# Optimization experiments

Measured on AMD Instinct MI355X. Metric: run time of the kernel, lower is better.

The kernel has to match this reference:

```python
import jax, jax.numpy as jnp
import numpy as np

B = 8            # graphs per batch
NUM_NODES = 12500  # nodes per graph
N = B * NUM_NODES  # 100000 total nodes
E = 1_600_000      # edges (avg degree 16)
F_IN = 128
HID = 128


def _glorot(key, shape):
    lim = np.sqrt(6.0 / (shape[0] + shape[1])).astype(np.float32)
    return jax.random.uniform(key, shape, jnp.float32, -lim, lim)


def setup_inputs() -> dict:
    key = jax.random.key(0)
    ks = jax.random.split(key, 8)
    x = jax.random.normal(ks[0], (N, F_IN), jnp.float32)
    edge_index = jax.random.randint(ks[1], (2, E), 0, N, jnp.int32)
    batch = jnp.repeat(jnp.arange(B, dtype=jnp.int32), NUM_NODES)
    W1 = _glorot(ks[2], (F_IN, HID)); b1 = jnp.zeros((HID,), jnp.float32)
    W2 = _glorot(ks[3], (HID, HID));  b2 = jnp.zeros((HID,), jnp.float32)
    W3 = _glorot(ks[4], (HID, 1));    b3 = jnp.zeros((1,), jnp.float32)
    return {"x": x, "edge_index": edge_index, "batch": batch,
            "W1": W1, "b1": b1, "W2": W2, "b2": b2, "W3": W3, "b3": b3}


def _gcn_norm(src, dst, n):
    """Add self-loops and compute symmetric D^-1/2 A D^-1/2 edge weights (PyG GCNConv default)."""
    loop = jnp.arange(n, dtype=src.dtype)
    s = jnp.concatenate([src, loop])
    d = jnp.concatenate([dst, loop])
    deg = jax.ops.segment_sum(jnp.ones(s.shape[0], jnp.float32), d, num_segments=n)
    dinv = jnp.where(deg > 0, jax.lax.rsqrt(deg), 0.0)
    return s, d, dinv[s] * dinv[d]


def _gcn_conv(h, W, b, s, d, norm, n):
    h = h @ W                                   # [n, out]
    msg = h[s] * norm[:, None]                  # gather + scale
    out = jax.ops.segment_sum(msg, d, num_segments=n)  # scatter-add
    return out + b


def reference(x, edge_index, batch, W1, b1, W2, b2, W3, b3):
    n = x.shape[0]
    x_last = x[:, -1]                           # == x.view(B,NUM_NODES,F)[:,:,-1] flattened
    s, d, norm = _gcn_norm(edge_index[0], edge_index[1], n)
    h = jax.nn.relu(_gcn_conv(x, W1, b1, s, d, norm, n))   # dropout is identity in eval mode
    h = jax.nn.relu(_gcn_conv(h, W2, b2, s, d, norm, n))
    h = jax.nn.relu(_gcn_conv(h, W3, b3, s, d, norm, n))   # [n, 1]
    x_res = h.reshape(B, NUM_NODES)
    return x_res + x_last.reshape(B, NUM_NODES)
```

## Files before the change

kernel.cpp:

```cpp
#include <hip/hip_runtime.h>
#include <hip/hip_bf16.h>

typedef __attribute__((ext_vector_type(8))) short short8;
typedef __attribute__((ext_vector_type(8))) __bf16 bf16x8;
typedef __attribute__((ext_vector_type(4))) float f32x4;

static __device__ __forceinline__ float bflo(unsigned u){ return __uint_as_float(u << 16); }
static __device__ __forceinline__ float bfhi(unsigned u){ return __uint_as_float(u & 0xffff0000u); }
static __device__ __forceinline__ unsigned short f2bf(float f){
  unsigned u = __float_as_uint(f);
  unsigned r = u + 0x7fffu + ((u >> 16) & 1u);
  return (unsigned short)(r >> 16);
}

#if __has_builtin(__builtin_amdgcn_cvt_pk_fp8_f32)
static __device__ __forceinline__ unsigned char f2e4m3(float f){
  return (unsigned char)(__builtin_amdgcn_cvt_pk_fp8_f32(f, 0.f, 0, false) & 0xff);
}
#else
static __device__ __forceinline__ unsigned char f2e4m3(float f){
  unsigned s = (__float_as_uint(f) >> 31) << 7;
  float a = fabsf(f);
  if (a >= 448.f) return (unsigned char)(s | 0x7e);
  if (a < 0.0009765625f) return (unsigned char)s;
  if (a >= 0.015625f){
    int e; float m = frexpf(a, &e);
    int q = (int)rintf(m * 16.f);
    int E = e - 1 + 7;
    if (q == 16){ q = 8; E++; }
    if (E >= 16) return (unsigned char)(s | 0x7e);
    return (unsigned char)(s | (E << 3) | (q - 8));
  } else {
    int q = (int)rintf(a * 512.f);
    if (q > 7) return (unsigned char)(s | 0x08);
    return (unsigned char)(s | q);
  }
}
#endif

#if __has_builtin(__builtin_amdgcn_cvt_pk_f32_fp8)
static __device__ __forceinline__ float4 e4m3x4_to_f32(unsigned u){
  auto lo = __builtin_amdgcn_cvt_pk_f32_fp8((int)u, false);
  auto hi = __builtin_amdgcn_cvt_pk_f32_fp8((int)u, true);
  return make_float4(lo[0], lo[1], hi[0], hi[1]);
}
#else
static __device__ __forceinline__ float e4m3_1(unsigned b){
  unsigned s = b >> 7, e = (b >> 3) & 15, m = b & 7;
  float v = e ? ldexpf((float)(8 + m) * 0.125f, (int)e - 7) : ldexpf((float)m * 0.125f, -6);
  return s ? -v : v;
}
static __device__ __forceinline__ float4 e4m3x4_to_f32(unsigned u){
  return make_float4(e4m3_1(u & 255), e4m3_1((u >> 8) & 255), e4m3_1((u >> 16) & 255), e4m3_1(u >> 24));
}
#endif

static __device__ __forceinline__ void add8(float* acc, uint2 u){
  float4 a = e4m3x4_to_f32(u.x), b = e4m3x4_to_f32(u.y);
  acc[0] += a.x; acc[1] += a.y; acc[2] += a.z; acc[3] += a.w;
  acc[4] += b.x; acc[5] += b.y; acc[6] += b.z; acc[7] += b.w;
}

#define NBMAX  1024
#define PART_C 4096
#define STCAP  4096
#define BCAP   6144


__global__ __launch_bounds__(1024) void k_part(const int* __restrict__ src, const int* __restrict__ dst,
    int* __restrict__ bpos, unsigned* __restrict__ ebuf, int E, int NB)
{
  __shared__ int hist[NBMAX + 1];
  __shared__ int hist2[NBMAX];
  __shared__ int gbase[NBMAX];
  __shared__ int sc[1024];
  __shared__ unsigned staged[PART_C];

  const int t = threadIdx.x;
  const int base = blockIdx.x * PART_C;

  for (int i = t; i < NBMAX; i += 1024){ hist[i] = 0; hist2[i] = 0; }
  __syncthreads();

  unsigned up[4];
  int bb[4];
  #pragma unroll
  for (int j = 0; j < 4; j++){
    int e = base + j * 1024 + t;
    if (e < E){
      int s = src[e], d = dst[e];
      bb[j] = d >> 7;
      up[j] = ((unsigned)s << 7) | (unsigned)(d & 127);
      atomicAdd(&hist[bb[j]], 1);
    } else bb[j] = -1;
  }
  __syncthreads();

  int v = (t < NB) ? hist[t] : 0;
  sc[t] = v; __syncthreads();
  for (int off = 1; off < 1024; off <<= 1){
    int u = (t >= off) ? sc[t - off] : 0;
    __syncthreads();
    sc[t] += u;
    __syncthreads();
  }
  int incl = sc[t];
  if (t < NB) hist[t] = incl - v;
  if (t == NB - 1) hist[NB] = incl;
  if (t < NB && v > 0) gbase[t] = t * BCAP + atomicAdd(&bpos[t], v);
  __syncthreads();

  #pragma unroll
  for (int j = 0; j < 4; j++){
    if (bb[j] >= 0){
      int r = atomicAdd(&hist2[bb[j]], 1);
      staged[hist[bb[j]] + r] = up[j];
    }
  }
  __syncthreads();

  int total = hist[NB];
  for (int i = t; i < total; i += 1024){
    int lo = 0, hi = NB;
    while (hi - lo > 1){
      int mid = (lo + hi) >> 1;
      if (hist[mid] <= i) lo = mid; else hi = mid;
    }
    ebuf[gbase[lo] + (i - hist[lo])] = staged[i];
  }
}

__global__ __launch_bounds__(1024) void k_cscan(const int* __restrict__ cnts, int* __restrict__ bstart,
    int* __restrict__ rowptr, int NB, int N, int E){
  __shared__ int sc[1024];
  const int t = threadIdx.x;
  int v = (t < NB) ? cnts[t] : 0;
  sc[t] = v; __syncthreads();
  for (int off = 1; off < 1024; off <<= 1){
    int u = (t >= off) ? sc[t - off] : 0;
    __syncthreads();
    sc[t] += u;
    __syncthreads();
  }
  if (t < NB) bstart[t] = sc[t] - v;
  if (t == 0){ bstart[NB] = E; rowptr[N] = E; }
}

__global__ __launch_bounds__(256) void k_bsort(const unsigned* __restrict__ ebuf, const int* __restrict__ cnts,
    const int* __restrict__ bstart, int* __restrict__ rowptr, int* __restrict__ colv,
    float* __restrict__ dinv, int n)
{
  __shared__ int cl[128];
  __shared__ int sc2[256];
  __shared__ unsigned stg[STCAP];

  const int t = threadIdx.x;
  const int b = blockIdx.x;
  const int r0 = b << 7;
  const int rbeg = b * BCAP;
  const int total = cnts[b];
  const int wbeg = bstart[b];

  if (t < 128) cl[t] = 0;
  __syncthreads();
  for (int i = t; i < total; i += 256) atomicAdd(&cl[ebuf[rbeg + i] & 127u], 1);
  __syncthreads();

  int v = (t < 128) ? cl[t] : 0;
  sc2[t] = v; __syncthreads();
  for (int off = 1; off < 256; off <<= 1){
    int u = (t >= off) ? sc2[t - off] : 0;
    __syncthreads();
    sc2[t] += u;
    __syncthreads();
  }
  int excl = sc2[t] - v;
  if (t < 128){
    int node = r0 + t;
    if (node < n){
      rowptr[node] = wbeg + excl;
      dinv[node]   = rsqrtf((float)(v + 1));
    }
    cl[t] = excl;
  }
  __syncthreads();

  if (total <= STCAP){
    for (int i = t; i < total; i += 256){
      unsigned u = ebuf[rbeg + i];
      int p = atomicAdd(&cl[u & 127u], 1);
      stg[p] = u >> 7;
    }
    __syncthreads();
    for (int i = t; i < total; i += 256) colv[wbeg + i] = (int)stg[i];
  } else {
    for (int i = t; i < total; i += 256){
      unsigned u = ebuf[rbeg + i];
      int p = atomicAdd(&cl[u & 127u], 1);
      colv[wbeg + p] = (int)(u >> 7);
    }
  }
}


template<bool AF32>
__global__ __launch_bounds__(512) void k_gemm_mfma(const void* __restrict__ Ain, const float* __restrict__ W,
    const float* __restrict__ dinv, unsigned char* __restrict__ G8, int n)
{
  __shared__ unsigned short At[128 * 136];
  __shared__ float dl[128];

  const int t = threadIdx.x;
  const int rowBase = blockIdx.x * 128;
  const int w  = t >> 6;
  const int l  = t & 63;
  const int ln = l & 15;
  const int lg = l >> 4;

  if (t < 128){
    int gr = rowBase + t;
    dl[t] = (gr < n) ? dinv[gr] : 0.f;
  }

  #pragma unroll
  for (int i = 0; i < 4; i++){
    int flat = i * 4096 + t * 8;
    int r = flat >> 7, c = flat & 127;
    int gr = rowBase + r;
    unsigned short tmp[8];
    if constexpr (AF32){
      const float* A = (const float*)Ain;
      float4 v0 = make_float4(0.f,0.f,0.f,0.f), v1 = v0;
      if (gr < n){
        v0 = *(const float4*)(A + (size_t)gr * 128 + c);
        v1 = *(const float4*)(A + (size_t)gr * 128 + c + 4);
      }
      tmp[0]=f2bf(v0.x); tmp[1]=f2bf(v0.y); tmp[2]=f2bf(v0.z); tmp[3]=f2bf(v0.w);
      tmp[4]=f2bf(v1.x); tmp[5]=f2bf(v1.y); tmp[6]=f2bf(v1.z); tmp[7]=f2bf(v1.w);
    } else {
      const unsigned short* A = (const unsigned short*)Ain;
      short8 v = {};
      if (gr < n) v = *(const short8*)(A + (size_t)gr * 128 + c);
      *(short8*)tmp = v;
    }
    int g = (c >> 3) ^ (r & 7);
    *(short8*)((char*)At + r * 256 + g * 16) = *(const short8*)tmp;
  }

  bf16x8 bfr[4];
  #pragma unroll
  for (int kk = 0; kk < 4; kk++){
    short8 tmp;
    #pragma unroll
    for (int j = 0; j < 8; j++){
      float wv = W[(kk * 32 + lg * 8 + j) * 128 + (w * 16 + ln)];
      tmp[j] = (short)f2bf(wv);
    }
    bfr[kk] = __builtin_bit_cast(bf16x8, tmp);
  }

  f32x4 acc[8];
  #pragma unroll
  for (int m = 0; m < 8; m++) acc[m] = (f32x4){0.f,0.f,0.f,0.f};

  __syncthreads();

  #pragma unroll
  for (int m = 0; m < 8; m++){
    int row = m * 16 + ln;
    #pragma unroll
    for (int kk = 0; kk < 4; kk++){
      int g = (kk * 4 + lg) ^ (row & 7);
      short8 av = *(const short8*)((const char*)At + row * 256 + g * 16);
      acc[m] = __builtin_amdgcn_mfma_f32_16x16x32_bf16(
          __builtin_bit_cast(bf16x8, av), bfr[kk], acc[m], 0, 0, 0);
    }
  }

  __syncthreads();
  unsigned char* At8 = (unsigned char*)At;

  #pragma unroll
  for (int m = 0; m < 8; m++){
    #pragma unroll
    for (int r = 0; r < 4; r++){
      int row = m * 16 + lg * 4 + r;
      At8[row * 136 + w * 16 + ln] = f2e4m3(dl[row] * acc[m][r]);
    }
  }
  __syncthreads();

  {
    int r = t >> 2, c = (t & 3) * 32;
    int gr = rowBase + r;
    if (gr < n){
      uint4 a = *(const uint4*)(At8 + r * 136 + c);
      uint4 b = *(const uint4*)(At8 + r * 136 + c + 16);
      *(uint4*)(G8 + (size_t)gr * 128 + c)      = a;
      *(uint4*)(G8 + (size_t)gr * 128 + c + 16) = b;
    }
  }
}


__global__ __launch_bounds__(256) void k_spmm(const uint2* __restrict__ G8, const int* __restrict__ rowptr,
    const int* __restrict__ colv, const float* __restrict__ dinv, const float* __restrict__ bias,
    unsigned* __restrict__ H, int n)
{
  int tid = blockIdx.x * 256 + threadIdx.x;
  int row = tid >> 4;
  int gl  = tid & 15;
  if (row >= n) return;

  float acc[8] = {0,0,0,0,0,0,0,0};
  add8(acc, G8[(size_t)row * 16 + gl]);
  int e = rowptr[row], e1 = rowptr[row + 1];

  for (; e + 8 <= e1; e += 8){
    int s0 = colv[e    ], s1 = colv[e + 1], s2 = colv[e + 2], s3 = colv[e + 3];
    int s4 = colv[e + 4], s5 = colv[e + 5], s6 = colv[e + 6], s7 = colv[e + 7];
    uint2 v0 = G8[(size_t)s0 * 16 + gl];
    uint2 v1 = G8[(size_t)s1 * 16 + gl];
    uint2 v2 = G8[(size_t)s2 * 16 + gl];
    uint2 v3 = G8[(size_t)s3 * 16 + gl];
    uint2 v4 = G8[(size_t)s4 * 16 + gl];
    uint2 v5 = G8[(size_t)s5 * 16 + gl];
    uint2 v6 = G8[(size_t)s6 * 16 + gl];
    uint2 v7 = G8[(size_t)s7 * 16 + gl];
    add8(acc, v0); add8(acc, v1); add8(acc, v2); add8(acc, v3);
    add8(acc, v4); add8(acc, v5); add8(acc, v6); add8(acc, v7);
  }
  for (; e + 4 <= e1; e += 4){
    int s0 = colv[e], s1 = colv[e + 1], s2 = colv[e + 2], s3 = colv[e + 3];
    uint2 v0 = G8[(size_t)s0 * 16 + gl];
    uint2 v1 = G8[(size_t)s1 * 16 + gl];
    uint2 v2 = G8[(size_t)s2 * 16 + gl];
    uint2 v3 = G8[(size_t)s3 * 16 + gl];
    add8(acc, v0); add8(acc, v1); add8(acc, v2); add8(acc, v3);
  }
  for (; e < e1; ++e) add8(acc, G8[(size_t)colv[e] * 16 + gl]);

  float dv = dinv[row];
  float4 b0 = *(const float4*)(bias + gl * 8);
  float4 b1 = *(const float4*)(bias + gl * 8 + 4);
  float r0 = fmaxf(fmaf(dv, acc[0], b0.x), 0.f);
  float r1 = fmaxf(fmaf(dv, acc[1], b0.y), 0.f);
  float r2 = fmaxf(fmaf(dv, acc[2], b0.z), 0.f);
  float r3 = fmaxf(fmaf(dv, acc[3], b0.w), 0.f);
  float r4 = fmaxf(fmaf(dv, acc[4], b1.x), 0.f);
  float r5 = fmaxf(fmaf(dv, acc[5], b1.y), 0.f);
  float r6 = fmaxf(fmaf(dv, acc[6], b1.z), 0.f);
  float r7 = fmaxf(fmaf(dv, acc[7], b1.w), 0.f);
  uint4 o;
  o.x = (unsigned)f2bf(r0) | ((unsigned)f2bf(r1) << 16);
  o.y = (unsigned)f2bf(r2) | ((unsigned)f2bf(r3) << 16);
  o.z = (unsigned)f2bf(r4) | ((unsigned)f2bf(r5) << 16);
  o.w = (unsigned)f2bf(r6) | ((unsigned)f2bf(r7) << 16);
  *(uint4*)(H + (size_t)row * 64 + gl * 4) = o;
}


__global__ __launch_bounds__(256) void k_gemv3(const unsigned* __restrict__ H, const float* __restrict__ W3,
    const float* __restrict__ dinv, float* __restrict__ tvec, int n)
{
  int wid  = (blockIdx.x * 256 + threadIdx.x) >> 6;
  int lane = threadIdx.x & 63;
  if (wid >= n) return;
  unsigned u = H[(size_t)wid * 64 + lane];
  float2 wv = *(const float2*)(W3 + lane * 2);
  float v = bflo(u) * wv.x + bfhi(u) * wv.y;
  #pragma unroll
  for (int off = 32; off; off >>= 1) v += __shfl_xor(v, off);
  if (lane == 0) tvec[wid] = dinv[wid] * v;
}

__global__ __launch_bounds__(256) void k_final3(const float* __restrict__ tvec, const int* __restrict__ rowptr,
    const int* __restrict__ colv, const float* __restrict__ dinv, const float* __restrict__ b3,
    const float* __restrict__ x, float* __restrict__ out, int n)
{
  int tid = blockIdx.x * 256 + threadIdx.x;
  int row = tid >> 4;
  int gl  = tid & 15;
  if (row >= n) return;
  float s = 0.f;
  int e0 = rowptr[row], e1 = rowptr[row + 1];
  for (int e = e0 + gl; e < e1; e += 16) s += tvec[colv[e]];
  s += __shfl_xor(s, 1); s += __shfl_xor(s, 2);
  s += __shfl_xor(s, 4); s += __shfl_xor(s, 8);
  if (gl == 0){
    s += tvec[row];
    float v = fmaxf(fmaf(dinv[row], s, b3[0]), 0.f);
    out[row] = v + x[(size_t)row * 128 + 127];
  }
}


extern "C" void kernel_launch(void* const* d_in, const int* in_sizes, int n_in,
                              void* d_out, int out_size, void* d_ws, size_t ws_size,
                              hipStream_t stream)
{
  const float* x  = (const float*)d_in[0];
  const int*   ei = (const int*)d_in[1];
  const float* W1 = (const float*)d_in[3];
  const float* b1 = (const float*)d_in[4];
  const float* W2 = (const float*)d_in[5];
  const float* b2 = (const float*)d_in[6];
  const float* W3 = (const float*)d_in[7];
  const float* b3 = (const float*)d_in[8];
  float* out = (float*)d_out;

  const int N = in_sizes[0] / 128;
  const int E = in_sizes[1] / 2;
  const int* src = ei;
  const int* dst = ei + E;
  const int NB = (N + 127) >> 7;

  char* wsb = (char*)d_ws;
  size_t off = 0;
  auto carve = [&](size_t bytes) -> void* {
    void* p = wsb + off;
    off += bytes;
    off = (off + 255) & ~(size_t)255;
    return p;
  };
  float*    dinv   = (float*)carve((size_t)N * 4);
  int*      rowptr = (int*)carve((size_t)(N + 1) * 4);
  int*      colv   = (int*)carve((size_t)E * 4);
  int*      bstart = (int*)carve((size_t)(NB + 1) * 4);
  int*      bpos   = (int*)carve((size_t)NB * 4);
  float*    tvec   = (float*)carve((size_t)N * 4);
  unsigned char* G8 = (unsigned char*)carve((size_t)N * 128);
  unsigned* H      = (unsigned*)carve((size_t)N * 256);
  unsigned* ebuf   = (unsigned*)H;

  hipMemsetAsync(bpos, 0, (size_t)NB * 4, stream);
  k_part  <<<(E + PART_C - 1) / PART_C, 1024, 0, stream>>>(src, dst, bpos, ebuf, E, NB);
  k_cscan <<<1, 1024, 0, stream>>>(bpos, bstart, rowptr, NB, N, E);
  k_bsort <<<NB, 256, 0, stream>>>(ebuf, bpos, bstart, rowptr, colv, dinv, N);

  k_gemm_mfma<true ><<<(N + 127) / 128, 512, 0, stream>>>(x, W1, dinv, G8, N);
  k_spmm<<<((size_t)N * 16 + 255) / 256, 256, 0, stream>>>((const uint2*)G8, rowptr, colv, dinv, b1, H, N);
  k_gemm_mfma<false><<<(N + 127) / 128, 512, 0, stream>>>(H, W2, dinv, G8, N);
  k_spmm<<<((size_t)N * 16 + 255) / 256, 256, 0, stream>>>((const uint2*)G8, rowptr, colv, dinv, b2, H, N);
  k_gemv3 <<<(N + 3) / 4, 256, 0, stream>>>(H, W3, dinv, tvec, N);
  k_final3<<<((size_t)N * 16 + 255) / 256, 256, 0, stream>>>(tvec, rowptr, colv, dinv, b3, x, out, N);
}
```

Measured before the change: 173.2 us.

## Widen SpMM gathers to 16 bytes and fuse layer-3 GEMV into second SpMM

The SpMM kernel now uses 8 threads per row, and each thread gathers 16 fp8 values through a uint4 load instead of 8 through a uint2. The second SpMM is templated to compute the W3 dot product directly and reduce it with shuffles, writing tvec. This removes the separate k_gemv3 launch and the write and re-read of the bf16 H matrix. Wider per-thread work means half as many threads and more registers per thread, which could lower occupancy and latency hiding on the gathers.

Result: faster. 167.6 us (-3.2%).

```diff
diff --git a/kernel.cpp b/kernel.cpp
--- a/kernel.cpp
+++ b/kernel.cpp
@@ -55,10 +55,13 @@
 }
 #endif
 
-static __device__ __forceinline__ void add8(float* acc, uint2 u){
-  float4 a = e4m3x4_to_f32(u.x), b = e4m3x4_to_f32(u.y);
-  acc[0] += a.x; acc[1] += a.y; acc[2] += a.z; acc[3] += a.w;
-  acc[4] += b.x; acc[5] += b.y; acc[6] += b.z; acc[7] += b.w;
+static __device__ __forceinline__ void add16(float* a, uint4 v){
+  float4 f0 = e4m3x4_to_f32(v.x), f1 = e4m3x4_to_f32(v.y);
+  float4 f2 = e4m3x4_to_f32(v.z), f3 = e4m3x4_to_f32(v.w);
+  a[0]+=f0.x; a[1]+=f0.y; a[2]+=f0.z; a[3]+=f0.w;
+  a[4]+=f1.x; a[5]+=f1.y; a[6]+=f1.z; a[7]+=f1.w;
+  a[8]+=f2.x; a[9]+=f2.y; a[10]+=f2.z; a[11]+=f2.w;
+  a[12]+=f3.x; a[13]+=f3.y; a[14]+=f3.z; a[15]+=f3.w;
 }
 
 #define NBMAX  1024
@@ -303,76 +306,91 @@
 }
 
 
-__global__ __launch_bounds__(256) void k_spmm(const uint2* __restrict__ G8, const int* __restrict__ rowptr,
+template<bool LAST>
+__global__ __launch_bounds__(256) void k_spmm(const uint4* __restrict__ G8, const int* __restrict__ rowptr,
     const int* __restrict__ colv, const float* __restrict__ dinv, const float* __restrict__ bias,
-    unsigned* __restrict__ H, int n)
+    const float* __restrict__ W3, unsigned* __restrict__ H, float* __restrict__ tvec, int n)
 {
   int tid = blockIdx.x * 256 + threadIdx.x;
-  int row = tid >> 4;
-  int gl  = tid & 15;
+  int row = tid >> 3;
+  int gl  = tid & 7;
   if (row >= n) return;
 
-  float acc[8] = {0,0,0,0,0,0,0,0};
-  add8(acc, G8[(size_t)row * 16 + gl]);
+  float acc[16] = {0,0,0,0,0,0,0,0,0,0,0,0,0,0,0,0};
+  add16(acc, G8[(size_t)row * 8 + gl]);
   int e = rowptr[row], e1 = rowptr[row + 1];
 
   for (; e + 8 <= e1; e += 8){
     int s0 = colv[e    ], s1 = colv[e + 1], s2 = colv[e + 2], s3 = colv[e + 3];
     int s4 = colv[e + 4], s5 = colv[e + 5], s6 = colv[e + 6], s7 = colv[e + 7];
-    uint2 v0 = G8[(size_t)s0 * 16 + gl];
-    uint2 v1 = G8[(size_t)s1 * 16 + gl];
-    uint2 v2 = G8[(size_t)s2 * 16 + gl];
-    uint2 v3 = G8[(size_t)s3 * 16 + gl];
-    uint2 v4 = G8[(size_t)s4 * 16 + gl];
-    uint2 v5 = G8[(size_t)s5 * 16 + gl];
-    uint2 v6 = G8[(size_t)s6 * 16 + gl];
-    uint2 v7 = G8[(size_t)s7 * 16 + gl];
-    add8(acc, v0); add8(acc, v1); add8(acc, v2); add8(acc, v3);
-    add8(acc, v4); add8(acc, v5); add8(acc, v6); add8(acc, v7);
+    uint4 v0 = G8[(size_t)s0 * 8 + gl];
+    uint4 v1 = G8[(size_t)s1 * 8 + gl];
+    uint4 v2 = G8[(size_t)s2 * 8 + gl];
+    uint4 v3 = G8[(size_t)s3 * 8 + gl];
+    uint4 v4 = G8[(size_t)s4 * 8 + gl];
+    uint4 v5 = G8[(size_t)s5 * 8 + gl];
+    uint4 v6 = G8[(size_t)s6 * 8 + gl];
+    uint4 v7 = G8[(size_t)s7 * 8 + gl];
+    add16(acc, v0); add16(acc, v1); add16(acc, v2); add16(acc, v3);
+    add16(acc, v4); add16(acc, v5); add16(acc, v6); add16(acc, v7);
   }
   for (; e + 4 <= e1; e += 4){
     int s0 = colv[e], s1 = colv[e + 1], s2 = colv[e + 2], s3 = colv[e + 3];
-    uint2 v0 = G8[(size_t)s0 * 16 + gl];
-    uint2 v1 = G8[(size_t)s1 * 16 + gl];
-    uint2 v2 = G8[(size_t)s2 * 16 + gl];
-    uint2 v3 = G8[(size_t)s3 * 16 + gl];
-    add8(acc, v0); add8(acc, v1); add8(acc, v2); add8(acc, v3);
-  }
-  for (; e < e1; ++e) add8(acc, G8[(size_t)colv[e] * 16 + gl]);
+    uint4 v0 = G8[(size_t)s0 * 8 + gl];
+    uint4 v1 = G8[(size_t)s1 * 8 + gl];
+    uint4 v2 = G8[(size_t)s2 * 8 + gl];
+    uint4 v3 = G8[(size_t)s3 * 8 + gl];
+    add16(acc, v0); add16(acc, v1); add16(acc, v2); add16(acc, v3);
+  }
+  for (; e < e1; ++e) add16(acc, G8[(size_t)colv[e] * 8 + gl]);
 
   float dv = dinv[row];
-  float4 b0 = *(const float4*)(bias + gl * 8);
-  float4 b1 = *(const float4*)(bias + gl * 8 + 4);
-  float r0 = fmaxf(fmaf(dv, acc[0], b0.x), 0.f);
-  float r1 = fmaxf(fmaf(dv, acc[1], b0.y), 0.f);
-  float r2 = fmaxf(fmaf(dv, acc[2], b0.z), 0.f);
-  float r3 = fmaxf(fmaf(dv, acc[3], b0.w), 0.f);
-  float r4 = fmaxf(fmaf(dv, acc[4], b1.x), 0.f);
-  float r5 = fmaxf(fmaf(dv, acc[5], b1.y), 0.f);
-  float r6 = fmaxf(fmaf(dv, acc[6], b1.z), 0.f);
-  float r7 = fmaxf(fmaf(dv, acc[7], b1.w), 0.f);
-  uint4 o;
-  o.x = (unsigned)f2bf(r0) | ((unsigned)f2bf(r1) << 16);
-  o.y = (unsigned)f2bf(r2) | ((unsigned)f2bf(r3) << 16);
-  o.z = (unsigned)f2bf(r4) | ((unsigned)f2bf(r5) << 16);
-  o.w = (unsigned)f2bf(r6) | ((unsigned)f2bf(r7) << 16);
-  *(uint4*)(H + (size_t)row * 64 + gl * 4) = o;
-}
-
-
-__global__ __launch_bounds__(256) void k_gemv3(const unsigned* __restrict__ H, const float* __restrict__ W3,
-    const float* __restrict__ dinv, float* __restrict__ tvec, int n)
-{
-  int wid  = (blockIdx.x * 256 + threadIdx.x) >> 6;
-  int lane = threadIdx.x & 63;
-  if (wid >= n) return;
-  unsigned u = H[(size_t)wid * 64 + lane];
-  float2 wv = *(const float2*)(W3 + lane * 2);
-  float v = bflo(u) * wv.x + bfhi(u) * wv.y;
-  #pragma unroll
-  for (int off = 32; off; off >>= 1) v += __shfl_xor(v, off);
-  if (lane == 0) tvec[wid] = dinv[wid] * v;
-}
+  float r[16];
+  {
+    const float4* bp = (const float4*)(bias + gl * 16);
+    float4 b0 = bp[0], b1 = bp[1], b2 = bp[2], b3 = bp[3];
+    r[0] = fmaxf(fmaf(dv, acc[0],  b0.x), 0.f);
+    r[1] = fmaxf(fmaf(dv, acc[1],  b0.y), 0.f);
+    r[2] = fmaxf(fmaf(dv, acc[2],  b0.z), 0.f);
+    r[3] = fmaxf(fmaf(dv, acc[3],  b0.w), 0.f);
+    r[4] = fmaxf(fmaf(dv, acc[4],  b1.x), 0.f);
+    r[5] = fmaxf(fmaf(dv, acc[5],  b1.y), 0.f);
+    r[6] = fmaxf(fmaf(dv, acc[6],  b1.z), 0.f);
+    r[7] = fmaxf(fmaf(dv, acc[7],  b1.w), 0.f);
+    r[8] = fmaxf(fmaf(dv, acc[8],  b2.x), 0.f);
+    r[9] = fmaxf(fmaf(dv, acc[9],  b2.y), 0.f);
+    r[10]= fmaxf(fmaf(dv, acc[10], b2.z), 0.f);
+    r[11]= fmaxf(fmaf(dv, acc[11], b2.w), 0.f);
+    r[12]= fmaxf(fmaf(dv, acc[12], b3.x), 0.f);
+    r[13]= fmaxf(fmaf(dv, acc[13], b3.y), 0.f);
+    r[14]= fmaxf(fmaf(dv, acc[14], b3.z), 0.f);
+    r[15]= fmaxf(fmaf(dv, acc[15], b3.w), 0.f);
+  }
+
+  if constexpr (!LAST){
+    uint4 o0, o1;
+    o0.x = (unsigned)f2bf(r[0])  | ((unsigned)f2bf(r[1])  << 16);
+    o0.y = (unsigned)f2bf(r[2])  | ((unsigned)f2bf(r[3])  << 16);
+    o0.z = (unsigned)f2bf(r[4])  | ((unsigned)f2bf(r[5])  << 16);
+    o0.w = (unsigned)f2bf(r[6])  | ((unsigned)f2bf(r[7])  << 16);
+    o1.x = (unsigned)f2bf(r[8])  | ((unsigned)f2bf(r[9])  << 16);
+    o1.y = (unsigned)f2bf(r[10]) | ((unsigned)f2bf(r[11]) << 16);
+    o1.z = (unsigned)f2bf(r[12]) | ((unsigned)f2bf(r[13]) << 16);
+    o1.w = (unsigned)f2bf(r[14]) | ((unsigned)f2bf(r[15]) << 16);
+    *(uint4*)(H + (size_t)row * 64 + gl * 8)     = o0;
+    *(uint4*)(H + (size_t)row * 64 + gl * 8 + 4) = o1;
+  } else {
+    const float4* wp = (const float4*)(W3 + gl * 16);
+    float4 w0 = wp[0], w1 = wp[1], w2 = wp[2], w3 = wp[3];
+    float s = r[0]*w0.x + r[1]*w0.y + r[2]*w0.z + r[3]*w0.w
+            + r[4]*w1.x + r[5]*w1.y + r[6]*w1.z + r[7]*w1.w
+            + r[8]*w2.x + r[9]*w2.y + r[10]*w2.z + r[11]*w2.w
+            + r[12]*w3.x + r[13]*w3.y + r[14]*w3.z + r[15]*w3.w;
+    s += __shfl_xor(s, 1); s += __shfl_xor(s, 2); s += __shfl_xor(s, 4);
+    if (gl == 0) tvec[row] = dv * s;
+  }
+}
+
 
 __global__ __launch_bounds__(256) void k_final3(const float* __restrict__ tvec, const int* __restrict__ rowptr,
     const int* __restrict__ colv, const float* __restrict__ dinv, const float* __restrict__ b3,
@@ -439,9 +457,8 @@
   k_bsort <<<NB, 256, 0, stream>>>(ebuf, bpos, bstart, rowptr, colv, dinv, N);
 
   k_gemm_mfma<true ><<<(N + 127) / 128, 512, 0, stream>>>(x, W1, dinv, G8, N);
-  k_spmm<<<((size_t)N * 16 + 255) / 256, 256, 0, stream>>>((const uint2*)G8, rowptr, colv, dinv, b1, H, N);
+  k_spmm<false><<<((size_t)N * 8 + 255) / 256, 256, 0, stream>>>((const uint4*)G8, rowptr, colv, dinv, b1, nullptr, H, nullptr, N);
   k_gemm_mfma<false><<<(N + 127) / 128, 512, 0, stream>>>(H, W2, dinv, G8, N);
-  k_spmm<<<((size_t)N * 16 + 255) / 256, 256, 0, stream>>>((const uint2*)G8, rowptr, colv, dinv, b2, H, N);
-  k_gemv3 <<<(N + 3) / 4, 256, 0, stream>>>(H, W3, dinv, tvec, N);
+  k_spmm<true ><<<((size_t)N * 8 + 255) / 256, 256, 0, stream>>>((const uint4*)G8, rowptr, colv, dinv, b2, W3, nullptr, tvec, N);
   k_final3<<<((size_t)N * 16 + 255) / 256, 256, 0, stream>>>(tvec, rowptr, colv, dinv, b3, x, out, N);
 }
```
